# Optimization experiments

Measured on AMD Instinct MI355X. Metric: run time of the kernel, lower is better.

The kernel has to match this reference:

```python
import jax, jax.numpy as jnp
import numpy as np

B, F, C, H, W = 256, 16, 256, 32, 32

def setup_inputs() -> dict:
    key = jax.random.key(0)
    kx, kk = jax.random.split(key)
    x = jax.random.normal(kx, (B, C, H, W), dtype=jnp.float32)
    # kaiming_normal init: std = sqrt(2 / fan_in), fan_in = C*H*W
    std = float(np.sqrt(2.0 / (C * H * W)))
    kernel = jax.random.normal(kk, (F, C, H, W), dtype=jnp.float32) * std
    return {"x": x, "kernel": kernel}

def reference(x, kernel):
    # (x[:,None] * kernel[None]).sum((-1,-2)) == einsum over spatial dims, per channel
    y = jnp.einsum('bchw,fchw->bfc', x, kernel)  # [B, F, C]
    return y.reshape(y.shape[0], -1)  # [B, F*C]
```

## Files before the change

kernel.cpp:

```cpp
#include <hip/hip_runtime.h>
#include <hip/hip_bf16.h>


constexpr int Bb = 256;
constexpr int Ff = 16;
constexpr int Cc = 256;
constexpr int HW = 1024;
constexpr int CHW = Cc * HW;

constexpr int BT = 64;
constexpr int RB = 2;
constexpr int NTHREADS = (BT / RB) * 16;
constexpr int NJ = HW / 4 / 16;

__device__ __forceinline__ float dot4(float4 a, float4 b) {
    return a.x * b.x + a.y * b.y + a.z * b.z + a.w * b.w;
}
__device__ __forceinline__ float red16(float v) {
    v += __shfl_xor(v, 1);
    v += __shfl_xor(v, 2);
    v += __shfl_xor(v, 4);
    v += __shfl_xor(v, 8);
    return v;
}

__global__ __launch_bounds__(NTHREADS)
void sle_kernel(const float* __restrict__ x, const float* __restrict__ k,
                float* __restrict__ out) {
    __shared__ float ldsK[Ff * HW];

    const int t   = threadIdx.x;
    const int thw = t & 15;
    const int tbg = t >> 4;

    const int g     = blockIdx.x;
    const int c     = (g & 7) * 32 + ((g >> 3) & 31);
    const int btile = g >> 8;
    const int b0    = btile * BT + tbg * RB;

    {
        const int fr = t >> 5, lane32 = t & 31;
        const float4* src = (const float4*)(k + (size_t)fr * CHW + (size_t)c * HW);
        float4* dst = (float4*)(ldsK + fr * HW);
#pragma unroll
        for (int q = 0; q < 8; ++q)
            dst[lane32 + 32 * q] = src[lane32 + 32 * q];
    }
    __syncthreads();

    const float* x0 = x + (size_t)(b0 + 0) * CHW + (size_t)c * HW;
    const float* x1 = x + (size_t)(b0 + 1) * CHW + (size_t)c * HW;

    float4 a00 = {0,0,0,0}, a01 = {0,0,0,0}, a02 = {0,0,0,0}, a03 = {0,0,0,0};
    float4 a10 = {0,0,0,0}, a11 = {0,0,0,0}, a12 = {0,0,0,0}, a13 = {0,0,0,0};

#pragma unroll 4
    for (int j = 0; j < NJ; ++j) {
        const int f4  = thw + 16 * j;
        const int off = 4 * f4;
        const float4 xv0 = *(const float4*)(x0 + off);
        const float4 xv1 = *(const float4*)(x1 + off);

#define ACC_G(G, A0, A1) {                                              \
        const float* kp = ldsK + (4 * (G)) * HW + off;                  \
        const float4 k0 = *(const float4*)(kp);                         \
        const float4 k1 = *(const float4*)(kp + HW);                    \
        const float4 k2 = *(const float4*)(kp + 2 * HW);                \
        const float4 k3 = *(const float4*)(kp + 3 * HW);                \
        A0.x += dot4(xv0, k0); A0.y += dot4(xv0, k1);                   \
        A0.z += dot4(xv0, k2); A0.w += dot4(xv0, k3);                   \
        A1.x += dot4(xv1, k0); A1.y += dot4(xv1, k1);                   \
        A1.z += dot4(xv1, k2); A1.w += dot4(xv1, k3); }

        ACC_G(0, a00, a10)
        ACC_G(1, a01, a11)
        ACC_G(2, a02, a12)
        ACC_G(3, a03, a13)
#undef ACC_G
    }

#define RED4(A) { A.x = red16(A.x); A.y = red16(A.y); \
                  A.z = red16(A.z); A.w = red16(A.w); }
    RED4(a00) RED4(a01) RED4(a02) RED4(a03)
    RED4(a10) RED4(a11) RED4(a12) RED4(a13)
#undef RED4

    __syncthreads();
    if (thw == 0) {
        float4* row0 = (float4*)(ldsK + (tbg * RB + 0) * Ff);
        float4* row1 = (float4*)(ldsK + (tbg * RB + 1) * Ff);
        row0[0] = a00; row0[1] = a01; row0[2] = a02; row0[3] = a03;
        row1[0] = a10; row1[1] = a11; row1[2] = a12; row1[3] = a13;
    }
    __syncthreads();

#pragma unroll
    for (int i = 0; i < (BT * Ff) / NTHREADS; ++i) {
        const int idx = t + NTHREADS * i;
        const int bl  = idx >> 4;
        const int f   = idx & 15;
        out[(size_t)(btile * BT + bl) * (Ff * Cc) + f * Cc + c] = ldsK[idx];
    }
}

extern "C" void kernel_launch(void* const* d_in, const int* in_sizes, int n_in,
                              void* d_out, int out_size, void* d_ws, size_t ws_size,
                              hipStream_t stream) {
    const float* x = (const float*)d_in[0];
    const float* k = (const float*)d_in[1];
    float* out = (float*)d_out;
    const int grid = Cc * (Bb / BT);
    sle_kernel<<<grid, NTHREADS, 0, stream>>>(x, k, out);
}
```

Measured before the change: 388.1 us.

## Process all batches per channel block with wave-wide reductions and one kernel load

The grid shrinks to one block per channel, with 512 threads (8 waves), each wave looping over 32 batches in groups of 4. This removes the 4x redundant loading of the 64KB kernel slice into LDS that the old batch-tiled grid required. Each lane now covers a whole 1024-element row via four float4 loads, reduces across all 64 lanes with shuffles, and writes its output through a select tree instead of an LDS round-trip. The cost is only 256 blocks for the GPU, which may limit occupancy and memory-level parallelism, plus a heavier 6-step shuffle reduction per batch group.

```diff
diff --git a/kernel.cpp b/kernel.cpp
--- a/kernel.cpp
+++ b/kernel.cpp
@@ -8,20 +8,17 @@
 constexpr int HW = 1024;
 constexpr int CHW = Cc * HW;
 
-constexpr int BT = 64;
-constexpr int RB = 2;
-constexpr int NTHREADS = (BT / RB) * 16;
-constexpr int NJ = HW / 4 / 16;
+constexpr int NTHREADS = 512;
+constexpr int WAVES = 8;
+constexpr int BPW = Bb / WAVES;
+constexpr int RB = 4;
+constexpr int NSI = BPW / RB;
 
 __device__ __forceinline__ float dot4(float4 a, float4 b) {
     return a.x * b.x + a.y * b.y + a.z * b.z + a.w * b.w;
 }
-__device__ __forceinline__ float red16(float v) {
-    v += __shfl_xor(v, 1);
-    v += __shfl_xor(v, 2);
-    v += __shfl_xor(v, 4);
-    v += __shfl_xor(v, 8);
-    return v;
+__device__ __forceinline__ float4 sel4(bool c, float4 a, float4 b) {
+    return c ? a : b;
 }
 
 __global__ __launch_bounds__(NTHREADS)
@@ -29,14 +26,12 @@
                 float* __restrict__ out) {
     __shared__ float ldsK[Ff * HW];
 
-    const int t   = threadIdx.x;
-    const int thw = t & 15;
-    const int tbg = t >> 4;
+    const int t    = threadIdx.x;
+    const int lane = t & 63;
+    const int w    = t >> 6;
 
-    const int g     = blockIdx.x;
-    const int c     = (g & 7) * 32 + ((g >> 3) & 31);
-    const int btile = g >> 8;
-    const int b0    = btile * BT + tbg * RB;
+    const int g = blockIdx.x;
+    const int c = (g & 7) * 32 + (g >> 3);
 
     {
         const int fr = t >> 5, lane32 = t & 31;
@@ -48,58 +43,79 @@
     }
     __syncthreads();
 
-    const float* x0 = x + (size_t)(b0 + 0) * CHW + (size_t)c * HW;
-    const float* x1 = x + (size_t)(b0 + 1) * CHW + (size_t)c * HW;
+    const float* xc   = x + (size_t)c * HW + 4 * lane;
+    float*       outc = out + c;
 
-    float4 a00 = {0,0,0,0}, a01 = {0,0,0,0}, a02 = {0,0,0,0}, a03 = {0,0,0,0};
-    float4 a10 = {0,0,0,0}, a11 = {0,0,0,0}, a12 = {0,0,0,0}, a13 = {0,0,0,0};
+    for (int si = 0; si < NSI; ++si) {
+        const int b0 = w * BPW + si * RB;
 
-#pragma unroll 4
-    for (int j = 0; j < NJ; ++j) {
-        const int f4  = thw + 16 * j;
-        const int off = 4 * f4;
-        const float4 xv0 = *(const float4*)(x0 + off);
-        const float4 xv1 = *(const float4*)(x1 + off);
+        float4 xv[RB][4];
+#pragma unroll
+        for (int s = 0; s < 4; ++s)
+#pragma unroll
+            for (int bb = 0; bb < RB; ++bb)
+                xv[bb][s] = *(const float4*)(xc + (size_t)(b0 + bb) * CHW + s * 256);
 
-#define ACC_G(G, A0, A1) {                                              \
-        const float* kp = ldsK + (4 * (G)) * HW + off;                  \
-        const float4 k0 = *(const float4*)(kp);                         \
-        const float4 k1 = *(const float4*)(kp + HW);                    \
-        const float4 k2 = *(const float4*)(kp + 2 * HW);                \
-        const float4 k3 = *(const float4*)(kp + 3 * HW);                \
-        A0.x += dot4(xv0, k0); A0.y += dot4(xv0, k1);                   \
-        A0.z += dot4(xv0, k2); A0.w += dot4(xv0, k3);                   \
-        A1.x += dot4(xv1, k0); A1.y += dot4(xv1, k1);                   \
-        A1.z += dot4(xv1, k2); A1.w += dot4(xv1, k3); }
-
-        ACC_G(0, a00, a10)
-        ACC_G(1, a01, a11)
-        ACC_G(2, a02, a12)
-        ACC_G(3, a03, a13)
-#undef ACC_G
-    }
-
-#define RED4(A) { A.x = red16(A.x); A.y = red16(A.y); \
-                  A.z = red16(A.z); A.w = red16(A.w); }
-    RED4(a00) RED4(a01) RED4(a02) RED4(a03)
-    RED4(a10) RED4(a11) RED4(a12) RED4(a13)
-#undef RED4
-
-    __syncthreads();
-    if (thw == 0) {
-        float4* row0 = (float4*)(ldsK + (tbg * RB + 0) * Ff);
-        float4* row1 = (float4*)(ldsK + (tbg * RB + 1) * Ff);
-        row0[0] = a00; row0[1] = a01; row0[2] = a02; row0[3] = a03;
-        row1[0] = a10; row1[1] = a11; row1[2] = a12; row1[3] = a13;
-    }
-    __syncthreads();
+        float4 a4[RB][4];
+#pragma unroll
+        for (int bb = 0; bb < RB; ++bb)
+#pragma unroll
+            for (int gg = 0; gg < 4; ++gg)
+                a4[bb][gg] = make_float4(0.f, 0.f, 0.f, 0.f);
 
 #pragma unroll
-    for (int i = 0; i < (BT * Ff) / NTHREADS; ++i) {
-        const int idx = t + NTHREADS * i;
-        const int bl  = idx >> 4;
-        const int f   = idx & 15;
-        out[(size_t)(btile * BT + bl) * (Ff * Cc) + f * Cc + c] = ldsK[idx];
+        for (int s = 0; s < 4; ++s) {
+            const float* kp = ldsK + s * 256 + 4 * lane;
+#pragma unroll
+            for (int gg = 0; gg < 4; ++gg) {
+                const float4 k0 = *(const float4*)(kp + (4 * gg + 0) * HW);
+                const float4 k1 = *(const float4*)(kp + (4 * gg + 1) * HW);
+                const float4 k2 = *(const float4*)(kp + (4 * gg + 2) * HW);
+                const float4 k3 = *(const float4*)(kp + (4 * gg + 3) * HW);
+#pragma unroll
+                for (int bb = 0; bb < RB; ++bb) {
+                    a4[bb][gg].x += dot4(xv[bb][s], k0);
+                    a4[bb][gg].y += dot4(xv[bb][s], k1);
+                    a4[bb][gg].z += dot4(xv[bb][s], k2);
+                    a4[bb][gg].w += dot4(xv[bb][s], k3);
+                }
+            }
+        }
+
+#pragma unroll
+        for (int bb = 0; bb < RB; ++bb)
+#pragma unroll
+            for (int gg = 0; gg < 4; ++gg) {
+                float4 v = a4[bb][gg];
+#pragma unroll
+                for (int m = 1; m <= 32; m <<= 1) {
+                    v.x += __shfl_xor(v.x, m);
+                    v.y += __shfl_xor(v.y, m);
+                    v.z += __shfl_xor(v.z, m);
+                    v.w += __shfl_xor(v.w, m);
+                }
+                a4[bb][gg] = v;
+            }
+
+        const int bsel = lane >> 4;
+        const int gsel = (lane >> 2) & 3;
+        const int csel = lane & 3;
+
+        const float4 vg0 = sel4(gsel & 2, sel4(gsel & 1, a4[0][3], a4[0][2]),
+                                          sel4(gsel & 1, a4[0][1], a4[0][0]));
+        const float4 vg1 = sel4(gsel & 2, sel4(gsel & 1, a4[1][3], a4[1][2]),
+                                          sel4(gsel & 1, a4[1][1], a4[1][0]));
+        const float4 vg2 = sel4(gsel & 2, sel4(gsel & 1, a4[2][3], a4[2][2]),
+                                          sel4(gsel & 1, a4[2][1], a4[2][0]));
+        const float4 vg3 = sel4(gsel & 2, sel4(gsel & 1, a4[3][3], a4[3][2]),
+                                          sel4(gsel & 1, a4[3][1], a4[3][0]));
+        const float4 vb  = sel4(bsel & 2, sel4(bsel & 1, vg3, vg2),
+                                          sel4(bsel & 1, vg1, vg0));
+        const float v01 = (csel & 1) ? vb.y : vb.x;
+        const float v23 = (csel & 1) ? vb.w : vb.z;
+        const float val = (csel & 2) ? v23 : v01;
+
+        outc[(size_t)(b0 + bsel) * (Ff * Cc) + (lane & 15) * Cc] = val;
     }
 }
 
@@ -109,6 +125,6 @@
     const float* x = (const float*)d_in[0];
     const float* k = (const float*)d_in[1];
     float* out = (float*)d_out;
-    const int grid = Cc * (Bb / BT);
+    const int grid = Cc;
     sle_kernel<<<grid, NTHREADS, 0, stream>>>(x, k, out);
 }
```

After: 494.9 us. 27.5% more time.
